# Performance work log

Hardware: AMD Instinct MI355X
Metric: run time of the kernel (lower is better)

The kernel has to match this reference:

```python
import jax, jax.numpy as jnp
import numpy as np

N_NODES = 50000
N_EDGES = 800000
C_IN = 128
HID = 128
C_OUT = 128


def _glorot(key, shape):
    fan_in, fan_out = shape
    lim = (6.0 / (fan_in + fan_out)) ** 0.5
    return jax.random.uniform(key, shape, jnp.float32, -lim, lim)


def setup_inputs() -> dict:
    key = jax.random.key(0)
    ks = jax.random.split(key, 8)
    x = jax.random.normal(ks[0], (N_NODES, C_IN), jnp.float32)
    edge_index = jax.random.randint(ks[1], (2, N_EDGES), 0, N_NODES, jnp.int32)
    return {
        "x": x,
        "edge_index": edge_index,
        # nn_in: Lin(2*C_IN, HID) -> ReLU -> Lin(HID, HID)
        "W1_in": _glorot(ks[2], (2 * C_IN, HID)), "b1_in": jnp.zeros((HID,), jnp.float32),
        "W2_in": _glorot(ks[3], (HID, HID)), "b2_in": jnp.zeros((HID,), jnp.float32),
        # nn_hid: Lin(2*HID, HID) -> ReLU -> Lin(HID, HID)
        "W1_hid": _glorot(ks[4], (2 * HID, HID)), "b1_hid": jnp.zeros((HID,), jnp.float32),
        "W2_hid": _glorot(ks[5], (HID, HID)), "b2_hid": jnp.zeros((HID,), jnp.float32),
        # nn_out: Lin(2*HID, HID) -> ReLU -> Lin(HID, C_OUT)
        "W1_out": _glorot(ks[6], (2 * HID, HID)), "b1_out": jnp.zeros((HID,), jnp.float32),
        "W2_out": _glorot(ks[7], (HID, C_OUT)), "b2_out": jnp.zeros((C_OUT,), jnp.float32),
    }


def _edge_conv(x, src, dst, W1, b1, W2, b2, n_nodes):
    # PyG EdgeConv: message = nn(concat(x_i, x_j - x_i)), aggr='max' over incoming edges
    xi = x[dst]                                   # [E, C] destination (center) nodes
    xj = x[src]                                   # [E, C] source (neighbor) nodes
    m = jnp.concatenate([xi, xj - xi], axis=-1)   # [E, 2C]
    h = jax.nn.relu(m @ W1 + b1) @ W2 + b2        # [E, H]
    agg = jax.ops.segment_max(h, dst, num_segments=n_nodes)  # [N, H]
    # PyG fills nodes with no incoming edges with 0 (segment_max yields -inf)
    return jnp.where(jnp.isfinite(agg), agg, 0.0)


def reference(x, edge_index, W1_in, b1_in, W2_in, b2_in,
              W1_hid, b1_hid, W2_hid, b2_hid,
              W1_out, b1_out, W2_out, b2_out):
    src, dst = edge_index[0], edge_index[1]
    n = x.shape[0]
    x = _edge_conv(x, src, dst, W1_in, b1_in, W2_in, b2_in, n)
    x = jax.nn.relu(x)
    x = _edge_conv(x, src, dst, W1_hid, b1_hid, W2_hid, b2_hid, n)
    x = jax.nn.relu(x)
    x = _edge_conv(x, src, dst, W1_out, b1_out, W2_out, b2_out, n)
    return x
```

## Files before the change

### kernel.cpp

```cpp
#include <hip/hip_runtime.h>

#define CH 128

typedef _Float16 f16;
typedef _Float16 f16x8 __attribute__((ext_vector_type(8)));
typedef float f32x4 __attribute__((ext_vector_type(4)));

__device__ __forceinline__ f32x4 mfma16(f16x8 a, f16x8 b, f32x4 c) {
    return __builtin_amdgcn_mfma_f32_16x16x32_f16(a, b, c, 0, 0, 0);
}

__global__ __launch_bounds__(256) void k_front(const int* __restrict__ edst, int* __restrict__ counts,
                                               int* __restrict__ erank, int E,
                                               const float* __restrict__ W1a, const float* __restrict__ W2a,
                                               const float* __restrict__ W1b, const float* __restrict__ W2b,
                                               const float* __restrict__ W1c, const float* __restrict__ W2c,
                                               f16* __restrict__ WcT, f16* __restrict__ W2T,
                                               const float* __restrict__ x, f16* __restrict__ act,
                                               int total4, int gHist) {
    int bid = blockIdx.x;
    if (bid < gHist) {
        int e = bid * 256 + threadIdx.x;
        if (e < E) erank[e] = atomicAdd(&counts[edst[e]], 1);
    } else if (bid < gHist + 576) {
        int r = bid - gHist;
        int l = r / 192;
        const float* W1 = (l == 0) ? W1a : (l == 1) ? W1b : W1c;
        const float* W2 = (l == 0) ? W2a : (l == 1) ? W2b : W2c;
        f16* wct = WcT + l * 256 * CH;
        f16* w2t = W2T + l * CH * CH;
        int id = (r % 192) * 256 + threadIdx.x;
        if (id < 32768) {
            int n = id >> 7, k = id & 127;
            float v;
            if (n < CH) v = W1[k * CH + n] - W1[(CH + k) * CH + n];
            else        v = W1[(CH + k) * CH + (n - CH)];
            wct[n * CH + k] = (f16)v;
        } else {
            int rr = id - 32768;
            int n = rr >> 7, k = rr & 127;
            w2t[n * CH + k] = (f16)W2[k * CH + n];
        }
    } else {
        int i = (bid - gHist - 576) * 256 + threadIdx.x;
        if (i < total4) {
            float4 v = ((const float4*)x)[i];
            f16 h0 = (f16)v.x, h1 = (f16)v.y, h2 = (f16)v.z, h3 = (f16)v.w;
            short4 s;
            s.x = *(short*)&h0; s.y = *(short*)&h1; s.z = *(short*)&h2; s.w = *(short*)&h3;
            ((short4*)act)[i] = s;
        }
    }
}

__global__ __launch_bounds__(256) void k_scan1(const int* __restrict__ counts, int* __restrict__ row_ptr,
                                               int* __restrict__ blockSums, int n) {
    __shared__ int s[256];
    int t = threadIdx.x;
    int i = blockIdx.x * 256 + t;
    s[t] = (i < n) ? counts[i] : 0;
    __syncthreads();
    for (int off = 1; off < 256; off <<= 1) {
        int x = (t >= off) ? s[t - off] : 0;
        __syncthreads();
        s[t] += x;
        __syncthreads();
    }
    if (i < n) row_ptr[i + 1] = s[t];
    if (t == 255) blockSums[blockIdx.x] = s[255];
}

__global__ __launch_bounds__(256) void k_scan2(const int* __restrict__ blockSums, int* __restrict__ blockOff, int nb) {
    __shared__ int s[256];
    int t = threadIdx.x;
    s[t] = (t < nb) ? blockSums[t] : 0;
    __syncthreads();
    for (int off = 1; off < 256; off <<= 1) {
        int x = (t >= off) ? s[t - off] : 0;
        __syncthreads();
        s[t] += x;
        __syncthreads();
    }
    blockOff[t] = (t == 0) ? 0 : s[t - 1];
}

__global__ __launch_bounds__(256) void k_scan3(int* __restrict__ row_ptr, const int* __restrict__ blockOff, int n) {
    int i = blockIdx.x * 256 + threadIdx.x;
    if (i < n) row_ptr[i + 1] += blockOff[blockIdx.x];
    if (blockIdx.x == 0 && threadIdx.x == 0) row_ptr[0] = 0;
}

__global__ __launch_bounds__(256) void k_scatter(const int* __restrict__ src, const int* __restrict__ dst,
                                                 const int* __restrict__ row_ptr, const int* __restrict__ erank,
                                                 int* __restrict__ sed, int E) {
    int e = blockIdx.x * 256 + threadIdx.x;
    if (e < E) {
        int pos = row_ptr[dst[e]] + erank[e];
        sed[pos] = src[e];
    }
}

__global__ __launch_bounds__(256) void k_gemm1(const f16* __restrict__ act, const f16* __restrict__ WcT,
                                               const float* __restrict__ b1,
                                               f16* __restrict__ P, f16* __restrict__ Q, int nrows) {
    int t = threadIdx.x;
    int w = t >> 6, lane = t & 63;
    int m = lane & 15, q = lane >> 4;
    int rowbase = blockIdx.x * 256 + w * 64;
    f16x8 a[4][4];
#pragma unroll
    for (int rt = 0; rt < 4; ++rt) {
        int rowc = min(rowbase + rt * 16 + m, nrows - 1);
#pragma unroll
        for (int kk = 0; kk < 4; ++kk)
            a[rt][kk] = *(const f16x8*)(act + (size_t)rowc * CH + kk * 32 + q * 8);
    }
#pragma unroll
    for (int nb = 0; nb < 16; ++nb) {
        f16x8 b[4];
#pragma unroll
        for (int kk = 0; kk < 4; ++kk)
            b[kk] = *(const f16x8*)(WcT + (nb * 16 + m) * CH + kk * 32 + q * 8);
        int col = nb * 16 + m;
        float bias = (nb < 8) ? b1[col] : 0.f;
#pragma unroll
        for (int rt = 0; rt < 4; ++rt) {
            f32x4 acc = {0.f, 0.f, 0.f, 0.f};
#pragma unroll
            for (int kk = 0; kk < 4; ++kk) acc = mfma16(a[rt][kk], b[kk], acc);
#pragma unroll
            for (int r = 0; r < 4; ++r) {
                int ro = rowbase + rt * 16 + q * 4 + r;
                if (ro < nrows) {
                    float v = acc[r] + bias;
                    if (nb < 8) P[(size_t)ro * CH + col] = (f16)v;
                    else        Q[(size_t)ro * CH + (col - CH)] = (f16)v;
                }
            }
        }
    }
}

__global__ __launch_bounds__(256, 3)
void k_node(const f16* __restrict__ P, const f16* __restrict__ Q,
            const f16* __restrict__ W2Tg, const float* __restrict__ b2,
            const int* __restrict__ row_ptr, const int* __restrict__ sed,
            f16* __restrict__ act_out, float* __restrict__ final_out,
            int n_nodes, int flags, int nwv) {
    __shared__ __align__(16) f16 w2lds[8 * 4 * 64 * 8];

    int t = threadIdx.x;
    int w = t >> 6, lane = t & 63;
    int m = lane & 15, q = lane >> 4;

#pragma unroll
    for (int i = t; i < 2048; i += 256) {
        int nb = i >> 8, rem = i & 255, kk = rem >> 6, ln = rem & 63;
        int mm = ln & 15, qq = ln >> 4;
        *(f16x8*)&w2lds[i * 8] = *(const f16x8*)(W2Tg + (size_t)(nb * 16 + mm) * CH + kk * 32 + qq * 8);
    }
    __syncthreads();

    float biasA = b2[lane], biasB = b2[lane + 64];
    const f16x8 z8 = {};
    const f32x4 z4 = {0.f, 0.f, 0.f, 0.f};

    auto mkAf = [&](const f16x8* pf, f16x8* qs) {
#pragma unroll
        for (int kk = 0; kk < 4; ++kk) qs[kk] = __builtin_elementwise_max(pf[kk] + qs[kk], z8);
    };
    auto tile1 = [&](const f16x8* af, float* rmax) {
        unsigned wo = 0;
        asm volatile("" : "+v"(wo));
        const f16* wb = w2lds + wo + (size_t)lane * 8;
#pragma unroll
        for (int nb = 0; nb < 8; ++nb) {
            f32x4 a0 = z4;
#pragma unroll
            for (int kk = 0; kk < 4; ++kk) {
                f16x8 bq = *(const f16x8*)(wb + (nb * 4 + kk) * 512);
                a0 = mfma16(af[kk], bq, a0);
            }
            rmax[nb] = fmaxf(fmaxf(fmaxf(a0[0], a0[1]), fmaxf(a0[2], a0[3])), rmax[nb]);
        }
    };
    auto tile2 = [&](const f16x8* af0, const f16x8* af1, float* rmax) {
        unsigned wo = 0;
        asm volatile("" : "+v"(wo));
        const f16* wb = w2lds + wo + (size_t)lane * 8;
#pragma unroll
        for (int nb = 0; nb < 8; ++nb) {
            f32x4 a0 = z4, a1 = z4;
#pragma unroll
            for (int kk = 0; kk < 4; ++kk) {
                f16x8 bq = *(const f16x8*)(wb + (nb * 4 + kk) * 512);
                a0 = mfma16(af0[kk], bq, a0);
                a1 = mfma16(af1[kk], bq, a1);
            }
            a0 = __builtin_elementwise_max(a0, a1);
            rmax[nb] = fmaxf(fmaxf(fmaxf(a0[0], a0[1]), fmaxf(a0[2], a0[3])), rmax[nb]);
        }
    };

    int nA = blockIdx.x * 4 + w;
    if (nA >= n_nodes) return;
    int nmax = n_nodes - 1;

    int rsA = row_ptr[nA], reA = row_ptr[nA + 1];
    int nB = nA + nwv; int nBc = min(nB, nmax);
    int rsB = row_ptr[nBc], reB = row_ptr[nBc + 1];
    int nC = nB + nwv; int nCc = min(nC, nmax);
    int rsC = row_ptr[nCc], reC = row_ptr[nCc + 1];

    int lA = (reA > rsA) ? reA - 1 : 0;
    int idx0A = sed[min(rsA + m, lA)];
    int idx1A = sed[min(rsA + 16 + m, lA)];
    int lB = (reB > rsB) ? reB - 1 : 0;
    int idx0B = sed[min(rsB + m, lB)];
    int idx1B = sed[min(rsB + 16 + m, lB)];

    f16x8 pfA[4], qs0A[4];
#pragma unroll
    for (int kk = 0; kk < 4; ++kk) {
        pfA[kk]  = *(const f16x8*)(P + (size_t)nA * CH + kk * 32 + q * 8);
        qs0A[kk] = *(const f16x8*)(Q + (size_t)idx0A * CH + kk * 32 + q * 8);
    }

    while (true) {
        f16x8 qs1A[4] = {};
        if (reA - rsA > 16) {
#pragma unroll
            for (int kk = 0; kk < 4; ++kk)
                qs1A[kk] = *(const f16x8*)(Q + (size_t)idx1A * CH + kk * 32 + q * 8);
        }
        f16x8 qs0B[4], pfB[4];
#pragma unroll
        for (int kk = 0; kk < 4; ++kk) {
            qs0B[kk] = *(const f16x8*)(Q + (size_t)idx0B * CH + kk * 32 + q * 8);
            pfB[kk]  = *(const f16x8*)(P + (size_t)nBc * CH + kk * 32 + q * 8);
        }
        int lC = (reC > rsC) ? reC - 1 : 0;
        int idx0C = sed[min(rsC + m, lC)];
        int idx1C = sed[min(rsC + 16 + m, lC)];
        int nD = nC + nwv; int nDc = min(nD, nmax);
        int rsD = row_ptr[nDc], reD = row_ptr[nDc + 1];

        float o0 = 0.f, o1 = 0.f;
        if (reA > rsA) {
            float rmax[8];
#pragma unroll
            for (int nb = 0; nb < 8; ++nb) rmax[nb] = -3.4e38f;
            mkAf(pfA, qs0A);
            if (reA - rsA > 16) {
                mkAf(pfA, qs1A);
                tile2(qs0A, qs1A, rmax);
            } else {
                tile1(qs0A, rmax);
            }
            for (int tb = rsA + 32; tb < reA; tb += 16) {
                int s2 = sed[min(tb + m, reA - 1)];
                f16x8 qx[4];
#pragma unroll
                for (int kk = 0; kk < 4; ++kk)
                    qx[kk] = *(const f16x8*)(Q + (size_t)s2 * CH + kk * 32 + q * 8);
                mkAf(pfA, qx);
                tile1(qx, rmax);
            }
#pragma unroll
            for (int nb = 0; nb < 8; ++nb) {
                float v = rmax[nb];
                v = fmaxf(v, __shfl_xor(v, 16));
                v = fmaxf(v, __shfl_xor(v, 32));
                rmax[nb] = v;
            }
            float vA = (q & 2) ? ((q & 1) ? rmax[3] : rmax[2]) : ((q & 1) ? rmax[1] : rmax[0]);
            float vB = (q & 2) ? ((q & 1) ? rmax[7] : rmax[6]) : ((q & 1) ? rmax[5] : rmax[4]);
            o0 = vA + biasA;
            o1 = vB + biasB;
            if (flags & 1) { o0 = fmaxf(o0, 0.f); o1 = fmaxf(o1, 0.f); }
        }
        if (flags & 2) {
            float* orow = final_out + (size_t)nA * CH;
            orow[lane] = o0; orow[lane + 64] = o1;
        } else {
            f16* orow = act_out + (size_t)nA * CH;
            orow[lane] = (f16)o0; orow[lane + 64] = (f16)o1;
        }

        if (nB >= n_nodes) break;

        nA = nB; rsA = rsB; reA = reB; idx1A = idx1B;
#pragma unroll
        for (int kk = 0; kk < 4; ++kk) { qs0A[kk] = qs0B[kk]; pfA[kk] = pfB[kk]; }
        idx0B = idx0C; idx1B = idx1C;
        nB = nC; nBc = nCc; rsB = rsC; reB = reC;
        nC = nD; nCc = nDc; rsC = rsD; reC = reD;
    }
}

extern "C" void kernel_launch(void* const* d_in, const int* in_sizes, int n_in,
                              void* d_out, int out_size, void* d_ws, size_t ws_size,
                              hipStream_t stream) {
    const float* x = (const float*)d_in[0];
    const int* ei  = (const int*)d_in[1];
    int E = in_sizes[1] / 2;
    int N = in_sizes[0] / CH;
    const int* esrc = ei;
    const int* edst = ei + E;

    const float* W1[3] = {(const float*)d_in[2], (const float*)d_in[6],  (const float*)d_in[10]};
    const float* B1[3] = {(const float*)d_in[3], (const float*)d_in[7],  (const float*)d_in[11]};
    const float* W2[3] = {(const float*)d_in[4], (const float*)d_in[8],  (const float*)d_in[12]};
    const float* B2[3] = {(const float*)d_in[5], (const float*)d_in[9],  (const float*)d_in[13]};

    char* base = (char*)d_ws;
    size_t off = 0;
    auto alloc = [&](size_t bytes) -> void* {
        void* p = base + off;
        off = (off + bytes + 255) & ~(size_t)255;
        return p;
    };
    int* counts    = (int*)alloc(sizeof(int) * (size_t)(N + 256));
    size_t zero_bytes = off;
    int* erank     = (int*)alloc(sizeof(int) * (size_t)E);
    int* row_ptr   = (int*)alloc(sizeof(int) * (size_t)(N + 1));
    int* blockSums = (int*)alloc(sizeof(int) * 256);
    int* blockOff  = (int*)alloc(sizeof(int) * 256);
    int* sed       = (int*)alloc(sizeof(int) * (size_t)E);
    f16* act       = (f16*)alloc(sizeof(f16) * (size_t)N * CH);
    f16* Pb        = (f16*)alloc(sizeof(f16) * (size_t)N * CH);
    f16* Qb        = (f16*)alloc(sizeof(f16) * (size_t)N * CH);
    f16* WcT       = (f16*)alloc(sizeof(f16) * 3 * 256 * CH);
    f16* W2T       = (f16*)alloc(sizeof(f16) * 3 * CH * CH);

    hipMemsetAsync(d_ws, 0, zero_bytes, stream);

    int gE = (E + 255) / 256;
    int gN = (N + 255) / 256;
    int total4 = N * CH / 4;
    int gCvt = (total4 + 255) / 256;
    k_front<<<gE + 576 + gCvt, 256, 0, stream>>>(edst, counts, erank, E,
                                                 W1[0], W2[0], W1[1], W2[1], W1[2], W2[2],
                                                 WcT, W2T, x, act, total4, gE);
    k_scan1<<<gN, 256, 0, stream>>>(counts, row_ptr, blockSums, N);
    k_scan2<<<1, 256, 0, stream>>>(blockSums, blockOff, gN);
    k_scan3<<<gN, 256, 0, stream>>>(row_ptr, blockOff, N);
    k_scatter<<<gE, 256, 0, stream>>>(esrc, edst, row_ptr, erank, sed, E);

    int gNode = 768;
    if (gNode > (N + 3) / 4) gNode = (N + 3) / 4;
    int nwv = gNode * 4;
    int gG1 = (N + 255) / 256;
    for (int l = 0; l < 3; ++l) {
        k_gemm1<<<gG1, 256, 0, stream>>>(act, WcT + l * 256 * CH, B1[l], Pb, Qb, N);
        int flags = (l < 2) ? 1 : 2;
        k_node<<<gNode, 256, 0, stream>>>(Pb, Qb, W2T + l * CH * CH, B2[l],
                                          row_ptr, sed, act, (float*)d_out, N, flags, nwv);
    }
}
```

Before: 388.2 us.

## Fuse three-pass scan into one kernel and merge scatter with first GEMM

Replaces the three scan kernels with a single-pass scan in which block 0 spin-waits on per-block flags, computes the block prefixes and publishes them back, so the other blocks pick up their carry without separate launches. The edge scatter into CSR order is merged into the same launch as the layer-0 node GEMM, using separate block ranges, so the two independent tasks run together. This removes three kernel launches and their serialization gaps. In exchange, the scan depends on all blocks being co-resident (gN≤256 here), since spin-waiting blocks could otherwise deadlock, and the flag array is cleared by the existing memset.

```diff
diff --git a/kernel.cpp b/kernel.cpp
--- a/kernel.cpp
+++ b/kernel.cpp
@@ -53,6 +53,58 @@
     }
 }
 
+__global__ __launch_bounds__(256) void k_scanOne(const int* __restrict__ counts, int* __restrict__ row_ptr,
+                                                 int* __restrict__ bsum, int* __restrict__ bpfx,
+                                                 int* __restrict__ bflag, int n, int nb) {
+    __shared__ int s[256];
+    __shared__ int carry;
+    int t = threadIdx.x, bid = blockIdx.x;
+    int i = bid * 256 + t;
+    s[t] = (i < n) ? counts[i] : 0;
+    __syncthreads();
+    for (int off = 1; off < 256; off <<= 1) {
+        int x = (t >= off) ? s[t - off] : 0;
+        __syncthreads();
+        s[t] += x;
+        __syncthreads();
+    }
+    int myIncl = s[t];
+    if (t == 255) {
+        __hip_atomic_store(&bsum[bid], myIncl, __ATOMIC_RELAXED, __HIP_MEMORY_SCOPE_AGENT);
+        __hip_atomic_store(&bflag[bid], 1, __ATOMIC_RELEASE, __HIP_MEMORY_SCOPE_AGENT);
+    }
+    if (bid == 0) {
+        int v = 0;
+        if (t < nb) {
+            int f;
+            do { f = __hip_atomic_load(&bflag[t], __ATOMIC_ACQUIRE, __HIP_MEMORY_SCOPE_AGENT); } while (f == 0);
+            v = __hip_atomic_load(&bsum[t], __ATOMIC_RELAXED, __HIP_MEMORY_SCOPE_AGENT);
+        }
+        __syncthreads();
+        s[t] = v;
+        __syncthreads();
+        for (int off = 1; off < 256; off <<= 1) {
+            int x = (t >= off) ? s[t - off] : 0;
+            __syncthreads();
+            s[t] += x;
+            __syncthreads();
+        }
+        int excl = (t == 0) ? 0 : s[t - 1];
+        if (t < nb) {
+            __hip_atomic_store(&bpfx[t], excl, __ATOMIC_RELAXED, __HIP_MEMORY_SCOPE_AGENT);
+            __hip_atomic_store(&bflag[t], 2, __ATOMIC_RELEASE, __HIP_MEMORY_SCOPE_AGENT);
+        }
+    }
+    if (t == 0) {
+        int f;
+        do { f = __hip_atomic_load(&bflag[bid], __ATOMIC_ACQUIRE, __HIP_MEMORY_SCOPE_AGENT); } while (f != 2);
+        carry = __hip_atomic_load(&bpfx[bid], __ATOMIC_RELAXED, __HIP_MEMORY_SCOPE_AGENT);
+    }
+    __syncthreads();
+    if (i < n) row_ptr[i + 1] = myIncl + carry;
+    if (bid == 0 && t == 0) row_ptr[0] = 0;
+}
+
 __global__ __launch_bounds__(256) void k_scan1(const int* __restrict__ counts, int* __restrict__ row_ptr,
                                                int* __restrict__ blockSums, int n) {
     __shared__ int s[256];
@@ -90,13 +142,56 @@
     if (blockIdx.x == 0 && threadIdx.x == 0) row_ptr[0] = 0;
 }
 
-__global__ __launch_bounds__(256) void k_scatter(const int* __restrict__ src, const int* __restrict__ dst,
-                                                 const int* __restrict__ row_ptr, const int* __restrict__ erank,
-                                                 int* __restrict__ sed, int E) {
-    int e = blockIdx.x * 256 + threadIdx.x;
-    if (e < E) {
-        int pos = row_ptr[dst[e]] + erank[e];
-        sed[pos] = src[e];
+__global__ __launch_bounds__(256) void k_scat_gemm(const f16* __restrict__ act, const f16* __restrict__ WcT,
+                                                   const float* __restrict__ b1,
+                                                   f16* __restrict__ P, f16* __restrict__ Q, int nrows, int gGemm,
+                                                   const int* __restrict__ src, const int* __restrict__ dst,
+                                                   const int* __restrict__ row_ptr, const int* __restrict__ erank,
+                                                   int* __restrict__ sed, int E) {
+    int bid = blockIdx.x;
+    if (bid < gGemm) {
+        int t = threadIdx.x;
+        int w = t >> 6, lane = t & 63;
+        int m = lane & 15, q = lane >> 4;
+        int rowbase = bid * 256 + w * 64;
+        f16x8 a[4][4];
+#pragma unroll
+        for (int rt = 0; rt < 4; ++rt) {
+            int rowc = min(rowbase + rt * 16 + m, nrows - 1);
+#pragma unroll
+            for (int kk = 0; kk < 4; ++kk)
+                a[rt][kk] = *(const f16x8*)(act + (size_t)rowc * CH + kk * 32 + q * 8);
+        }
+#pragma unroll
+        for (int nb = 0; nb < 16; ++nb) {
+            f16x8 b[4];
+#pragma unroll
+            for (int kk = 0; kk < 4; ++kk)
+                b[kk] = *(const f16x8*)(WcT + (nb * 16 + m) * CH + kk * 32 + q * 8);
+            int col = nb * 16 + m;
+            float bias = (nb < 8) ? b1[col] : 0.f;
+#pragma unroll
+            for (int rt = 0; rt < 4; ++rt) {
+                f32x4 acc = {0.f, 0.f, 0.f, 0.f};
+#pragma unroll
+                for (int kk = 0; kk < 4; ++kk) acc = mfma16(a[rt][kk], b[kk], acc);
+#pragma unroll
+                for (int r = 0; r < 4; ++r) {
+                    int ro = rowbase + rt * 16 + q * 4 + r;
+                    if (ro < nrows) {
+                        float v = acc[r] + bias;
+                        if (nb < 8) P[(size_t)ro * CH + col] = (f16)v;
+                        else        Q[(size_t)ro * CH + (col - CH)] = (f16)v;
+                    }
+                }
+            }
+        }
+    } else {
+        int e = (bid - gGemm) * 256 + threadIdx.x;
+        if (e < E) {
+            int pos = row_ptr[dst[e]] + erank[e];
+            sed[pos] = src[e];
+        }
     }
 }
 
@@ -321,7 +416,10 @@
         return p;
     };
     int* counts    = (int*)alloc(sizeof(int) * (size_t)(N + 256));
+    int* bflag     = (int*)alloc(sizeof(int) * 256);
     size_t zero_bytes = off;
+    int* bsum      = (int*)alloc(sizeof(int) * 256);
+    int* bpfx      = (int*)alloc(sizeof(int) * 256);
     int* erank     = (int*)alloc(sizeof(int) * (size_t)E);
     int* row_ptr   = (int*)alloc(sizeof(int) * (size_t)(N + 1));
     int* blockSums = (int*)alloc(sizeof(int) * 256);
@@ -342,16 +440,24 @@
     k_front<<<gE + 576 + gCvt, 256, 0, stream>>>(edst, counts, erank, E,
                                                  W1[0], W2[0], W1[1], W2[1], W1[2], W2[2],
                                                  WcT, W2T, x, act, total4, gE);
-    k_scan1<<<gN, 256, 0, stream>>>(counts, row_ptr, blockSums, N);
-    k_scan2<<<1, 256, 0, stream>>>(blockSums, blockOff, gN);
-    k_scan3<<<gN, 256, 0, stream>>>(row_ptr, blockOff, N);
-    k_scatter<<<gE, 256, 0, stream>>>(esrc, edst, row_ptr, erank, sed, E);
+    if (gN <= 256) {
+        k_scanOne<<<gN, 256, 0, stream>>>(counts, row_ptr, bsum, bpfx, bflag, N, gN);
+    } else {
+        k_scan1<<<gN, 256, 0, stream>>>(counts, row_ptr, blockSums, N);
+        k_scan2<<<1, 256, 0, stream>>>(blockSums, blockOff, gN);
+        k_scan3<<<gN, 256, 0, stream>>>(row_ptr, blockOff, N);
+    }
 
     int gNode = 768;
     if (gNode > (N + 3) / 4) gNode = (N + 3) / 4;
     int nwv = gNode * 4;
     int gG1 = (N + 255) / 256;
-    for (int l = 0; l < 3; ++l) {
+
+    k_scat_gemm<<<gG1 + gE, 256, 0, stream>>>(act, WcT, B1[0], Pb, Qb, N, gG1,
+                                              esrc, edst, row_ptr, erank, sed, E);
+    k_node<<<gNode, 256, 0, stream>>>(Pb, Qb, W2T, B2[0],
+                                      row_ptr, sed, act, (float*)d_out, N, 1, nwv);
+    for (int l = 1; l < 3; ++l) {
         k_gemm1<<<gG1, 256, 0, stream>>>(act, WcT + l * 256 * CH, B1[l], Pb, Qb, N);
         int flags = (l < 2) ? 1 : 2;
         k_node<<<gNode, 256, 0, stream>>>(Pb, Qb, W2T + l * CH * CH, B2[l],
```

Result: slower. 403.2 us (+3.9%).
